# Optimization experiments

Hardware: AMD Instinct MI355X
Metric: run time of the kernel (lower is better)

Reference implementation:

```python
import jax, jax.numpy as jnp
import numpy as np

N, E, F_IN, HID, K, CLS = 50000, 800000, 512, 128, 4, 40
EPS = 0.3


def setup_inputs() -> dict:
    key = jax.random.key(0)
    ks = jax.random.split(key, 6)
    x = jax.random.normal(ks[0], (N, F_IN), dtype=jnp.float32)
    edge_index = jax.random.randint(ks[1], (2, E), 0, N, dtype=jnp.int32)
    # xavier_normal with gain=1.414 ~ gain*sqrt(2/(fan_in+fan_out))
    t1_w = jax.random.normal(ks[2], (HID, F_IN), jnp.float32) * (1.414 * np.sqrt(2.0 / (F_IN + HID)))
    t1_b = jnp.zeros((HID,), jnp.float32)
    gate_w = jax.random.normal(ks[3], (K, 2 * HID), jnp.float32) * (1.414 * np.sqrt(2.0 / (2 * HID + 1)))
    gate_b = jnp.zeros((K,), jnp.float32)
    t2_w = jax.random.normal(ks[4], (CLS, HID), jnp.float32) * (1.414 * np.sqrt(2.0 / (HID + CLS)))
    t2_b = jnp.zeros((CLS,), jnp.float32)
    return dict(x=x, edge_index=edge_index, t1_w=t1_w, t1_b=t1_b,
                gate_w=gate_w, gate_b=gate_b, t2_w=t2_w, t2_b=t2_b)


def _fa_layer(h, row, col, nd, gw, gb):
    # gate(cat[h_row, h_col]) as two matvecs (equivalent to concat + Linear)
    d = h.shape[1]
    g = jnp.tanh(h[row] @ gw[:d] + h[col] @ gw[d:] + gb)   # [E]
    norm = g * nd[row] * nd[col]                           # [E]
    msg = norm[:, None] * h[row]                           # x_j = h[source], [E, HID]
    # aggregate (add) into target nodes
    return jax.ops.segment_sum(msg, col, num_segments=h.shape[0])


def reference(x, edge_index, t1_w, t1_b, gate_w, gate_b, t2_w, t2_b):
    row, col = edge_index[0], edge_index[1]
    deg = jax.ops.segment_sum(jnp.ones((E,), x.dtype), row, num_segments=N)
    nd = jnp.clip(deg, 1.0, None) ** -0.5                  # degree^{-1/2}, clamped at 1
    h = jax.nn.relu(x @ t1_w.T + t1_b)                     # [N, HID]
    raw = h
    for k in range(K):
        h = EPS * raw + _fa_layer(h, row, col, nd, gate_w[k], gate_b[k])
    return jax.nn.log_softmax(h @ t2_w.T + t2_b, axis=1)   # [N, CLS]
```

## Files before the change

kernel.cpp:

```cpp
#include <hip/hip_runtime.h>
#include <math.h>

#define N_NODES 50000
#define N_EDGES 800000
#define F_IN    512
#define HID     128
#define K_LAYERS 4
#define N_CLS   40
#define EPS_C   0.3f
#define CAP     64

typedef __bf16 bf16x8 __attribute__((ext_vector_type(8)));
typedef float  f32x4  __attribute__((ext_vector_type(4)));

__device__ inline unsigned short bfb(float f) {
    __bf16 b = (__bf16)f;
    return __builtin_bit_cast(unsigned short, b);
}
__device__ inline unsigned pack2(float a, float b) {
    return (unsigned)bfb(a) | ((unsigned)bfb(b) << 16);
}
__device__ inline float lo2(unsigned v) { return __builtin_bit_cast(float, v << 16); }
__device__ inline float hi2(unsigned v) { return __builtin_bit_cast(float, v & 0xffff0000u); }
__device__ inline bf16x8 ld_frag(const unsigned short* p) {
    uint4 q = *(const uint4*)p;
    return __builtin_bit_cast(bf16x8, q);
}

__global__ void k_prep(const int* __restrict__ row, const int* __restrict__ col,
                       int* __restrict__ deg, int* __restrict__ cur,
                       int* __restrict__ bucket) {
    int e = blockIdx.x * blockDim.x + threadIdx.x;
    if (e < N_EDGES) {
        int r = row[e], c = col[e];
        atomicAdd(&deg[r], 1);
        int p = atomicAdd(&cur[c], 1);
        if (p < CAP) bucket[((size_t)c << 6) + p] = r;
    }
}

__global__ void k_nd(const int* __restrict__ deg, float* __restrict__ nd) {
    int i = blockIdx.x * blockDim.x + threadIdx.x;
    if (i < N_NODES) {
        float d = fmaxf((float)deg[i], 1.0f);
        nd[i] = 1.0f / sqrtf(d);
    }
}

#define GS 72
__global__ __launch_bounds__(256) void k_gemm_mfma(const float* __restrict__ x,
                                                   const float* __restrict__ w,
                                                   const float* __restrict__ bias,
                                                   float* __restrict__ h0) {
    __shared__ __attribute__((aligned(16))) unsigned short As[128 * GS];
    __shared__ __attribute__((aligned(16))) unsigned short Bs[128 * GS];
    const int t    = threadIdx.x;
    const int lane = t & 63;
    const int wv   = t >> 6;
    const int wrow = wv >> 1;
    const int wcol = wv & 1;
    const int nb0  = blockIdx.x * 128;
    const int m16  = lane & 15;
    const int quad = lane >> 4;

    f32x4 acc[4][4];
#pragma unroll
    for (int mi = 0; mi < 4; mi++)
#pragma unroll
        for (int ni = 0; ni < 4; ni++) acc[mi][ni] = (f32x4){0.f, 0.f, 0.f, 0.f};

    for (int k0 = 0; k0 < F_IN; k0 += 64) {
        __syncthreads();
        {
            int r  = t & 127;
            int kh = (t >> 7) * 32;
            int n  = nb0 + r;
            unsigned short* pl = &As[r * GS + kh];
            if (n < N_NODES) {
                const float* px = &x[(size_t)n * F_IN + k0 + kh];
#pragma unroll
                for (int q = 0; q < 4; q++) {
                    float4 f0 = *(const float4*)(px + q * 8);
                    float4 f1 = *(const float4*)(px + q * 8 + 4);
                    *(ushort4*)(pl + q * 8)     = make_ushort4(bfb(f0.x), bfb(f0.y), bfb(f0.z), bfb(f0.w));
                    *(ushort4*)(pl + q * 8 + 4) = make_ushort4(bfb(f1.x), bfb(f1.y), bfb(f1.z), bfb(f1.w));
                }
            } else {
#pragma unroll
                for (int q = 0; q < 8; q++) *(ushort4*)(pl + q * 4) = make_ushort4(0, 0, 0, 0);
            }
        }
        {
            int j  = t & 127;
            int kh = (t >> 7) * 32;
            const float* pw = &w[(size_t)j * F_IN + k0 + kh];
            unsigned short* pl = &Bs[j * GS + kh];
#pragma unroll
            for (int q = 0; q < 4; q++) {
                float4 f0 = *(const float4*)(pw + q * 8);
                float4 f1 = *(const float4*)(pw + q * 8 + 4);
                *(ushort4*)(pl + q * 8)     = make_ushort4(bfb(f0.x), bfb(f0.y), bfb(f0.z), bfb(f0.w));
                *(ushort4*)(pl + q * 8 + 4) = make_ushort4(bfb(f1.x), bfb(f1.y), bfb(f1.z), bfb(f1.w));
            }
        }
        __syncthreads();
#pragma unroll
        for (int kk = 0; kk < 64; kk += 32) {
            bf16x8 af[4], bfr[4];
#pragma unroll
            for (int mi = 0; mi < 4; mi++)
                af[mi] = ld_frag(&As[(wrow * 64 + mi * 16 + m16) * GS + kk + quad * 8]);
#pragma unroll
            for (int ni = 0; ni < 4; ni++)
                bfr[ni] = ld_frag(&Bs[(wcol * 64 + ni * 16 + m16) * GS + kk + quad * 8]);
#pragma unroll
            for (int mi = 0; mi < 4; mi++)
#pragma unroll
                for (int ni = 0; ni < 4; ni++)
                    acc[mi][ni] = __builtin_amdgcn_mfma_f32_16x16x32_bf16(af[mi], bfr[ni], acc[mi][ni], 0, 0, 0);
        }
    }
    float bj[4];
#pragma unroll
    for (int ni = 0; ni < 4; ni++) bj[ni] = bias[wcol * 64 + ni * 16 + m16];
#pragma unroll
    for (int mi = 0; mi < 4; mi++)
#pragma unroll
        for (int reg = 0; reg < 4; reg++) {
            int n = nb0 + wrow * 64 + mi * 16 + quad * 4 + reg;
            if (n < N_NODES) {
#pragma unroll
                for (int ni = 0; ni < 4; ni++)
                    h0[(size_t)n * HID + wcol * 64 + ni * 16 + m16] =
                        fmaxf(acc[mi][ni][reg] + bj[ni], 0.f);
            }
        }
}

__global__ __launch_bounds__(256) void k_h2b_ab(const float* __restrict__ raw,
                                                const float* __restrict__ nd,
                                                const float* __restrict__ gw,
                                                unsigned* __restrict__ h0b,
                                                float2* __restrict__ pn0,
                                                float* __restrict__ bn0) {
    const int node = blockIdx.x * 4 + (threadIdx.x >> 6);
    const int lane = threadIdx.x & 63;
    if (node >= N_NODES) return;
    float2 hv = ((const float2*)raw)[((size_t)node << 6) + lane];
    h0b[((size_t)node << 6) + lane] = pack2(hv.x, hv.y);
    float pa = hv.x * gw[2 * lane]       + hv.y * gw[2 * lane + 1];
    float pb = hv.x * gw[128 + 2 * lane] + hv.y * gw[129 + 2 * lane];
#pragma unroll
    for (int d = 32; d > 0; d >>= 1) {
        pa += __shfl_xor(pa, d);
        pb += __shfl_xor(pb, d);
    }
    if (lane == 0) { pn0[node] = make_float2(pa, nd[node]); bn0[node] = pb; }
}

__global__ __launch_bounds__(256) void k_agg5(const unsigned* __restrict__ hb,
                                              const float* __restrict__ raw,
                                              const float2* __restrict__ pn,
                                              const float* __restrict__ bn,
                                              const int* __restrict__ bucket,
                                              const int* __restrict__ cur,
                                              const float* __restrict__ gb_all, int k,
                                              unsigned* __restrict__ outb,
                                              const float* __restrict__ gwn,
                                              float2* __restrict__ pnn,
                                              float* __restrict__ bnn) {
    const int node = blockIdx.x * 4 + (threadIdx.x >> 6);
    const int lane = threadIdx.x & 63;
    if (node >= N_NODES) return;
    const int cnt = min(cur[node], CAP);
    const float ndc = pn[node].y;
    const float bw  = bn[node] + gb_all[k];
    float2 rv = *(const float2*)&raw[((size_t)node << 7) + 2 * lane];
    float acc0 = EPS_C * rv.x;
    float acc1 = EPS_C * rv.y;

    int   idx = 0;
    float g   = 0.f;
    if (lane < cnt) {
        idx = bucket[((size_t)node << 6) + lane];
        float2 pr = pn[idx];
        g = tanhf(pr.x + bw) * pr.y * ndc;
    }

    int i = 0;
    for (; i + 4 <= cnt; i += 4) {
        int   r0 = __shfl(idx, i);     float g0 = __shfl(g, i);
        int   r1 = __shfl(idx, i + 1); float g1 = __shfl(g, i + 1);
        int   r2 = __shfl(idx, i + 2); float g2 = __shfl(g, i + 2);
        int   r3 = __shfl(idx, i + 3); float g3 = __shfl(g, i + 3);
        unsigned v0 = hb[((size_t)r0 << 6) + lane];
        unsigned v1 = hb[((size_t)r1 << 6) + lane];
        unsigned v2 = hb[((size_t)r2 << 6) + lane];
        unsigned v3 = hb[((size_t)r3 << 6) + lane];
        acc0 = fmaf(g0, lo2(v0), acc0); acc1 = fmaf(g0, hi2(v0), acc1);
        acc0 = fmaf(g1, lo2(v1), acc0); acc1 = fmaf(g1, hi2(v1), acc1);
        acc0 = fmaf(g2, lo2(v2), acc0); acc1 = fmaf(g2, hi2(v2), acc1);
        acc0 = fmaf(g3, lo2(v3), acc0); acc1 = fmaf(g3, hi2(v3), acc1);
    }
    for (; i < cnt; i++) {
        int   r  = __shfl(idx, i);
        float gg = __shfl(g, i);
        unsigned v = hb[((size_t)r << 6) + lane];
        acc0 = fmaf(gg, lo2(v), acc0);
        acc1 = fmaf(gg, hi2(v), acc1);
    }
    outb[((size_t)node << 6) + lane] = pack2(acc0, acc1);

    if (gwn) {
        float pa = acc0 * gwn[2 * lane]       + acc1 * gwn[2 * lane + 1];
        float pb = acc0 * gwn[128 + 2 * lane] + acc1 * gwn[129 + 2 * lane];
#pragma unroll
        for (int d = 32; d > 0; d >>= 1) {
            pa += __shfl_xor(pa, d);
            pb += __shfl_xor(pb, d);
        }
        if (lane == 0) { pnn[node] = make_float2(pa, ndc); bnn[node] = pb; }
    }
}

__global__ __launch_bounds__(256) void k_out(const unsigned* __restrict__ hb,
                                             const float* __restrict__ w2,
                                             const float* __restrict__ b2,
                                             float* __restrict__ out) {
    __shared__ float ws[N_CLS][HID + 1];
    __shared__ float hs[4][HID];
    __shared__ float bs[N_CLS];
    const int t = threadIdx.x;
    for (int i = t; i < N_CLS * HID; i += 256) {
        ws[i / HID][i % HID] = w2[i];
    }
    if (t < N_CLS) bs[t] = b2[t];
    int wv = t >> 6, lane = t & 63;
    int node = blockIdx.x * 4 + wv;
    if (node < N_NODES) {
        unsigned v = hb[((size_t)node << 6) + lane];
        hs[wv][2 * lane]     = lo2(v);
        hs[wv][2 * lane + 1] = hi2(v);
    }
    __syncthreads();
    float z = -INFINITY;
    if (node < N_NODES && lane < N_CLS) {
        float s = bs[lane];
#pragma unroll 8
        for (int kk = 0; kk < HID; kk++) s = fmaf(hs[wv][kk], ws[lane][kk], s);
        z = s;
    }
    float mx = z;
#pragma unroll
    for (int d = 32; d > 0; d >>= 1) mx = fmaxf(mx, __shfl_xor(mx, d));
    float ex = (z == -INFINITY) ? 0.f : expf(z - mx);
    float sum = ex;
#pragma unroll
    for (int d = 32; d > 0; d >>= 1) sum += __shfl_xor(sum, d);
    if (node < N_NODES && lane < N_CLS)
        out[(size_t)node * N_CLS + lane] = z - mx - logf(sum);
}

extern "C" void kernel_launch(void* const* d_in, const int* in_sizes, int n_in,
                              void* d_out, int out_size, void* d_ws, size_t ws_size,
                              hipStream_t stream) {
    const float* x   = (const float*)d_in[0];
    const int*   ei  = (const int*)d_in[1];
    const float* t1w = (const float*)d_in[2];
    const float* t1b = (const float*)d_in[3];
    const float* gw  = (const float*)d_in[4];
    const float* gb  = (const float*)d_in[5];
    const float* t2w = (const float*)d_in[6];
    const float* t2b = (const float*)d_in[7];
    float* out = (float*)d_out;

    const int* row = ei;
    const int* col = ei + N_EDGES;

    char* p = (char*)d_ws;
    auto alloc = [&](size_t bytes) -> char* {
        char* q = p;
        p += (bytes + 255) & ~(size_t)255;
        return q;
    };
    float*    raw    = (float*)alloc(sizeof(float) * (size_t)N_NODES * HID);
    unsigned* h0b    = (unsigned*)alloc(sizeof(unsigned) * (size_t)N_NODES * 64);
    unsigned* hA     = (unsigned*)alloc(sizeof(unsigned) * (size_t)N_NODES * 64);
    unsigned* hB     = (unsigned*)alloc(sizeof(unsigned) * (size_t)N_NODES * 64);
    float2*   pn0    = (float2*)alloc(sizeof(float2) * N_NODES);
    float2*   pn1    = (float2*)alloc(sizeof(float2) * N_NODES);
    float*    bn0    = (float*)alloc(sizeof(float) * N_NODES);
    float*    bn1    = (float*)alloc(sizeof(float) * N_NODES);
    float*    nd     = (float*)alloc(sizeof(float) * N_NODES);
    int*      degi   = (int*)alloc(sizeof(int) * N_NODES);
    int*      cur    = (int*)alloc(sizeof(int) * N_NODES);
    int*      bucket = (int*)alloc(sizeof(int) * (size_t)N_NODES * CAP);

    hipMemsetAsync(degi, 0, sizeof(int) * N_NODES, stream);
    hipMemsetAsync(cur,  0, sizeof(int) * N_NODES, stream);

    const int eb = (N_EDGES + 255) / 256;
    const int nb = (N_NODES + 255) / 256;
    const int wb = (N_NODES + 3) / 4;

    k_prep<<<eb, 256, 0, stream>>>(row, col, degi, cur, bucket);
    k_nd<<<nb, 256, 0, stream>>>(degi, nd);

    k_gemm_mfma<<<(N_NODES + 127) / 128, 256, 0, stream>>>(x, t1w, t1b, raw);
    k_h2b_ab<<<wb, 256, 0, stream>>>(raw, nd, gw, h0b, pn0, bn0);

    const unsigned* hc = h0b;
    unsigned* ring[2] = {hA, hB};
    const float2* pc = pn0;  float2* pnx = pn1;
    const float*  bc = bn0;  float*  bnx = bn1;
    for (int k = 0; k < K_LAYERS; k++) {
        unsigned* hn = ring[k & 1];
        const float* gwn = (k + 1 < K_LAYERS) ? (gw + (size_t)(k + 1) * 2 * HID) : nullptr;
        k_agg5<<<wb, 256, 0, stream>>>(hc, raw, pc, bc, bucket, cur, gb, k, hn, gwn, pnx, bnx);
        hc = hn;
        const float2* tp = pc; pc = pnx; pnx = (float2*)tp;
        const float*  tb = bc; bc = bnx; bnx = (float*)tb;
    }

    k_out<<<wb, 256, 0, stream>>>(hc, t2w, t2b, out);
}
```

Measured before the change: 470.1 us.

## Fuse edge bucketing into GEMM kernel and vectorize aggregation with 16-byte gathers

The edge-bucketing prep kernel is removed and its work moved to the start of the input GEMM kernel, with each block handling 2048 edges. This saves one launch and lets the atomic traffic overlap with GEMM work. The aggregation kernel now splits each wave into four 16-lane groups, so each group gathers a neighbour row with 16-byte loads and a wave processes 8 edges per iteration. Partial sums are then reduced across the groups with cross-lane shuffles. This cuts gather instruction count per edge, but adds shuffle reductions and makes the GEMM blocks wait on atomics first.

New measurement: 457.3 us. 1.03x faster.

```diff
diff --git a/kernel.cpp b/kernel.cpp
--- a/kernel.cpp
+++ b/kernel.cpp
@@ -27,18 +27,6 @@
     return __builtin_bit_cast(bf16x8, q);
 }
 
-__global__ void k_prep(const int* __restrict__ row, const int* __restrict__ col,
-                       int* __restrict__ deg, int* __restrict__ cur,
-                       int* __restrict__ bucket) {
-    int e = blockIdx.x * blockDim.x + threadIdx.x;
-    if (e < N_EDGES) {
-        int r = row[e], c = col[e];
-        atomicAdd(&deg[r], 1);
-        int p = atomicAdd(&cur[c], 1);
-        if (p < CAP) bucket[((size_t)c << 6) + p] = r;
-    }
-}
-
 __global__ void k_nd(const int* __restrict__ deg, float* __restrict__ nd) {
     int i = blockIdx.x * blockDim.x + threadIdx.x;
     if (i < N_NODES) {
@@ -48,10 +36,30 @@
 }
 
 #define GS 72
+#define EPB 2048
 __global__ __launch_bounds__(256) void k_gemm_mfma(const float* __restrict__ x,
                                                    const float* __restrict__ w,
                                                    const float* __restrict__ bias,
-                                                   float* __restrict__ h0) {
+                                                   float* __restrict__ h0,
+                                                   const int* __restrict__ row,
+                                                   const int* __restrict__ col,
+                                                   int* __restrict__ deg,
+                                                   int* __restrict__ cur,
+                                                   int* __restrict__ bucket) {
+    {
+        int e0 = blockIdx.x * EPB + threadIdx.x;
+#pragma unroll
+        for (int q = 0; q < EPB / 256; q++) {
+            int e = e0 + q * 256;
+            if (e < N_EDGES) {
+                int r = row[e], c = col[e];
+                atomicAdd(&deg[r], 1);
+                int p = atomicAdd(&cur[c], 1);
+                if (p < CAP) bucket[((size_t)c << 6) + p] = r;
+            }
+        }
+    }
+
     __shared__ __attribute__((aligned(16))) unsigned short As[128 * GS];
     __shared__ __attribute__((aligned(16))) unsigned short Bs[128 * GS];
     const int t    = threadIdx.x;
@@ -158,7 +166,7 @@
     if (lane == 0) { pn0[node] = make_float2(pa, nd[node]); bn0[node] = pb; }
 }
 
-__global__ __launch_bounds__(256) void k_agg5(const unsigned* __restrict__ hb,
+__global__ __launch_bounds__(256) void k_agg6(const unsigned* __restrict__ hb,
                                               const float* __restrict__ raw,
                                               const float2* __restrict__ pn,
                                               const float* __restrict__ bn,
@@ -172,12 +180,11 @@
     const int node = blockIdx.x * 4 + (threadIdx.x >> 6);
     const int lane = threadIdx.x & 63;
     if (node >= N_NODES) return;
-    const int cnt = min(cur[node], CAP);
+    const int esub = lane >> 4;
+    const int fg   = lane & 15;
+    const int cnt  = min(cur[node], CAP);
     const float ndc = pn[node].y;
     const float bw  = bn[node] + gb_all[k];
-    float2 rv = *(const float2*)&raw[((size_t)node << 7) + 2 * lane];
-    float acc0 = EPS_C * rv.x;
-    float acc1 = EPS_C * rv.y;
 
     int   idx = 0;
     float g   = 0.f;
@@ -187,35 +194,61 @@
         g = tanhf(pr.x + bw) * pr.y * ndc;
     }
 
-    int i = 0;
-    for (; i + 4 <= cnt; i += 4) {
-        int   r0 = __shfl(idx, i);     float g0 = __shfl(g, i);
-        int   r1 = __shfl(idx, i + 1); float g1 = __shfl(g, i + 1);
-        int   r2 = __shfl(idx, i + 2); float g2 = __shfl(g, i + 2);
-        int   r3 = __shfl(idx, i + 3); float g3 = __shfl(g, i + 3);
-        unsigned v0 = hb[((size_t)r0 << 6) + lane];
-        unsigned v1 = hb[((size_t)r1 << 6) + lane];
-        unsigned v2 = hb[((size_t)r2 << 6) + lane];
-        unsigned v3 = hb[((size_t)r3 << 6) + lane];
-        acc0 = fmaf(g0, lo2(v0), acc0); acc1 = fmaf(g0, hi2(v0), acc1);
-        acc0 = fmaf(g1, lo2(v1), acc0); acc1 = fmaf(g1, hi2(v1), acc1);
-        acc0 = fmaf(g2, lo2(v2), acc0); acc1 = fmaf(g2, hi2(v2), acc1);
-        acc0 = fmaf(g3, lo2(v3), acc0); acc1 = fmaf(g3, hi2(v3), acc1);
-    }
-    for (; i < cnt; i++) {
-        int   r  = __shfl(idx, i);
-        float gg = __shfl(g, i);
-        unsigned v = hb[((size_t)r << 6) + lane];
-        acc0 = fmaf(gg, lo2(v), acc0);
-        acc1 = fmaf(gg, hi2(v), acc1);
-    }
-    outb[((size_t)node << 6) + lane] = pack2(acc0, acc1);
+    float acc[8];
+#pragma unroll
+    for (int j = 0; j < 8; j++) acc[j] = 0.f;
+
+    const uint4* hb4 = (const uint4*)hb;
+    for (int base = 0; base < cnt; base += 8) {
+        int p0 = base + esub;
+        int p1 = p0 + 4;
+        int   e0 = __shfl(idx, p0);
+        int   e1 = __shfl(idx, p1);
+        float g0 = __shfl(g, p0);
+        float g1 = __shfl(g, p1);
+        uint4 v0 = hb4[(size_t)e0 * 16 + fg];
+        uint4 v1 = hb4[(size_t)e1 * 16 + fg];
+        acc[0] = fmaf(g0, lo2(v0.x), acc[0]); acc[1] = fmaf(g0, hi2(v0.x), acc[1]);
+        acc[2] = fmaf(g0, lo2(v0.y), acc[2]); acc[3] = fmaf(g0, hi2(v0.y), acc[3]);
+        acc[4] = fmaf(g0, lo2(v0.z), acc[4]); acc[5] = fmaf(g0, hi2(v0.z), acc[5]);
+        acc[6] = fmaf(g0, lo2(v0.w), acc[6]); acc[7] = fmaf(g0, hi2(v0.w), acc[7]);
+        acc[0] = fmaf(g1, lo2(v1.x), acc[0]); acc[1] = fmaf(g1, hi2(v1.x), acc[1]);
+        acc[2] = fmaf(g1, lo2(v1.y), acc[2]); acc[3] = fmaf(g1, hi2(v1.y), acc[3]);
+        acc[4] = fmaf(g1, lo2(v1.z), acc[4]); acc[5] = fmaf(g1, hi2(v1.z), acc[5]);
+        acc[6] = fmaf(g1, lo2(v1.w), acc[6]); acc[7] = fmaf(g1, hi2(v1.w), acc[7]);
+    }
+
+#pragma unroll
+    for (int j = 0; j < 8; j++) {
+        acc[j] += __shfl_xor(acc[j], 16);
+        acc[j] += __shfl_xor(acc[j], 32);
+    }
+
+    const float4* raw4 = (const float4*)raw;
+    float4 r0 = raw4[(size_t)node * 32 + 2 * fg];
+    float4 r1 = raw4[(size_t)node * 32 + 2 * fg + 1];
+    float of[8];
+    of[0] = fmaf(EPS_C, r0.x, acc[0]); of[1] = fmaf(EPS_C, r0.y, acc[1]);
+    of[2] = fmaf(EPS_C, r0.z, acc[2]); of[3] = fmaf(EPS_C, r0.w, acc[3]);
+    of[4] = fmaf(EPS_C, r1.x, acc[4]); of[5] = fmaf(EPS_C, r1.y, acc[5]);
+    of[6] = fmaf(EPS_C, r1.z, acc[6]); of[7] = fmaf(EPS_C, r1.w, acc[7]);
+    if (esub == 0) {
+        uint4 ov;
+        ov.x = pack2(of[0], of[1]); ov.y = pack2(of[2], of[3]);
+        ov.z = pack2(of[4], of[5]); ov.w = pack2(of[6], of[7]);
+        ((uint4*)outb)[(size_t)node * 16 + fg] = ov;
+    }
 
     if (gwn) {
-        float pa = acc0 * gwn[2 * lane]       + acc1 * gwn[2 * lane + 1];
-        float pb = acc0 * gwn[128 + 2 * lane] + acc1 * gwn[129 + 2 * lane];
-#pragma unroll
-        for (int d = 32; d > 0; d >>= 1) {
+        const float4* gw4 = (const float4*)gwn;
+        float4 wa0 = gw4[fg * 2], wa1 = gw4[fg * 2 + 1];
+        float4 wb0 = gw4[32 + fg * 2], wb1 = gw4[32 + fg * 2 + 1];
+        float pa = of[0] * wa0.x + of[1] * wa0.y + of[2] * wa0.z + of[3] * wa0.w
+                 + of[4] * wa1.x + of[5] * wa1.y + of[6] * wa1.z + of[7] * wa1.w;
+        float pb = of[0] * wb0.x + of[1] * wb0.y + of[2] * wb0.z + of[3] * wb0.w
+                 + of[4] * wb1.x + of[5] * wb1.y + of[6] * wb1.z + of[7] * wb1.w;
+#pragma unroll
+        for (int d = 1; d <= 8; d <<= 1) {
             pa += __shfl_xor(pa, d);
             pb += __shfl_xor(pb, d);
         }
@@ -299,14 +332,13 @@
     hipMemsetAsync(degi, 0, sizeof(int) * N_NODES, stream);
     hipMemsetAsync(cur,  0, sizeof(int) * N_NODES, stream);
 
-    const int eb = (N_EDGES + 255) / 256;
     const int nb = (N_NODES + 255) / 256;
     const int wb = (N_NODES + 3) / 4;
-
-    k_prep<<<eb, 256, 0, stream>>>(row, col, degi, cur, bucket);
+    const int gb_blocks = (N_NODES + 127) / 128;
+
+    k_gemm_mfma<<<gb_blocks, 256, 0, stream>>>(x, t1w, t1b, raw,
+                                               row, col, degi, cur, bucket);
     k_nd<<<nb, 256, 0, stream>>>(degi, nd);
-
-    k_gemm_mfma<<<(N_NODES + 127) / 128, 256, 0, stream>>>(x, t1w, t1b, raw);
     k_h2b_ab<<<wb, 256, 0, stream>>>(raw, nd, gw, h0b, pn0, bn0);
 
     const unsigned* hc = h0b;
@@ -316,7 +348,7 @@
     for (int k = 0; k < K_LAYERS; k++) {
         unsigned* hn = ring[k & 1];
         const float* gwn = (k + 1 < K_LAYERS) ? (gw + (size_t)(k + 1) * 2 * HID) : nullptr;
-        k_agg5<<<wb, 256, 0, stream>>>(hc, raw, pc, bc, bucket, cur, gb, k, hn, gwn, pnx, bnx);
+        k_agg6<<<wb, 256, 0, stream>>>(hc, raw, pc, bc, bucket, cur, gb, k, hn, gwn, pnx, bnx);
         hc = hn;
         const float2* tp = pc; pc = pnx; pnx = (float2*)tp;
         const float*  tb = bc; bc = bnx; bnx = (float*)tb;
```
